# Performance work log

Measured on AMD Instinct MI355X. Metric: run time of the kernel, lower is better.

The kernel has to match this reference:

```python
import jax, jax.numpy as jnp
import numpy as np

N = 20000   # total nodes (all graphs flattened)
E = 640000  # total edges
D = 512     # num_node_features
H = 512     # hidden_channels
G = 64      # number of graphs in the batch


def setup_inputs() -> dict:
    key = jax.random.key(0)
    ks = jax.random.split(key, 12)
    s = 0.05
    return {
        "x_a": jax.random.normal(ks[0], (N, D), dtype=jnp.float32),
        "edge_index_a": jax.random.randint(ks[1], (2, E), 0, N),
        "batch_a": jnp.sort(jax.random.randint(ks[2], (N,), 0, G)),
        "x_b": jax.random.normal(ks[3], (N, D), dtype=jnp.float32),
        "edge_index_b": jax.random.randint(ks[4], (2, E), 0, N),
        "batch_b": jnp.sort(jax.random.randint(ks[5], (N,), 0, G)),
        "W1": jax.random.normal(ks[6], (D, H), dtype=jnp.float32) * s,
        "b1": jnp.zeros((H,), dtype=jnp.float32),
        "W2": jax.random.normal(ks[7], (H, H), dtype=jnp.float32) * s,
        "b2": jnp.zeros((H,), dtype=jnp.float32),
        "W3": jax.random.normal(ks[8], (H, H), dtype=jnp.float32) * s,
        "b3": jnp.zeros((H,), dtype=jnp.float32),
    }


def _gcn_conv(x, src, dst, W, b, n):
    # GCNConv with self-loops and symmetric normalization:
    # out = D^{-1/2} (A + I) D^{-1/2} X W + b,  deg_i = 1 + in_degree(i)
    h = x @ W                                                  # [n, H]
    deg = jax.ops.segment_sum(jnp.ones((src.shape[0],), h.dtype), dst,
                              num_segments=n) + 1.0            # self-loop
    dinv = jax.lax.rsqrt(deg)                                  # deg^{-1/2}
    norm = dinv[src] * dinv[dst]                               # [E]
    agg = jax.ops.segment_sum(h[src] * norm[:, None], dst, num_segments=n)
    agg = agg + h * (dinv * dinv)[:, None]                     # self-loop term
    return agg + b


def _encode(x, edge_index, batch, W1, b1, W2, b2, W3, b3):
    src, dst = edge_index[0], edge_index[1]
    n = x.shape[0]
    h = jax.nn.relu(_gcn_conv(x, src, dst, W1, b1, n))
    h = jax.nn.relu(_gcn_conv(h, src, dst, W2, b2, n))
    h = _gcn_conv(h, src, dst, W3, b3, n)
    # global mean pool over graphs
    sums = jax.ops.segment_sum(h, batch, num_segments=G)       # [G, H]
    cnts = jax.ops.segment_sum(jnp.ones((n,), h.dtype), batch, num_segments=G)
    return sums / jnp.maximum(cnts, 1.0)[:, None]


def reference(x_a, edge_index_a, batch_a, x_b, edge_index_b, batch_b,
              W1, b1, W2, b2, W3, b3):
    out_a = _encode(x_a, edge_index_a, batch_a, W1, b1, W2, b2, W3, b3)
    out_b = _encode(x_b, edge_index_b, batch_b, W1, b1, W2, b2, W3, b3)
    # torch F.pairwise_distance: ||a - b + eps||_2 with eps=1e-6
    return jnp.linalg.norm(out_a - out_b + 1e-6, axis=-1)      # [G]
```

## Files before the change

kernel.cpp:

```cpp
#include <hip/hip_runtime.h>
#include <hip/hip_fp16.h>


typedef short bf16x8 __attribute__((ext_vector_type(8)));
typedef float f32x4 __attribute__((ext_vector_type(4)));

__device__ __forceinline__ unsigned short f2bf(float f) {
    union { float f; unsigned u; } v; v.f = f;
    unsigned r = (v.u + 0x7fffu + ((v.u >> 16) & 1u)) >> 16;
    return (unsigned short)r;
}
__device__ __forceinline__ float bf2f(unsigned short h) {
    union { unsigned u; float f; } v; v.u = ((unsigned)h) << 16;
    return v.f;
}

__device__ __forceinline__ void gload16(const unsigned short* g, unsigned short* lds) {
    __builtin_amdgcn_global_load_lds(
        (const __attribute__((address_space(1))) unsigned int*)g,
        (__attribute__((address_space(3))) unsigned int*)lds, 16, 0, 0);
}


__global__ __launch_bounds__(256) void deg2_kernel(const int* __restrict__ ei_a,
                                                   const int* __restrict__ ei_b,
                                                   int* __restrict__ deg,
                                                   int n, int e) {
    int i = blockIdx.x * 256 + threadIdx.x;
    if (i >= 2 * e) return;
    if (i < e) {
        atomicAdd(&deg[ei_a[e + i]], 1);
    } else {
        atomicAdd(&deg[n + ei_b[e + (i - e)]], 1);
    }
}

__global__ __launch_bounds__(1024) void scan2_kernel(const int* __restrict__ deg_all,
                                                     int* __restrict__ rp_all,
                                                     int* __restrict__ cur_all,
                                                     float* __restrict__ dinv_all, int n) {
    int enc = blockIdx.x;
    const int* deg = deg_all + (size_t)enc * n;
    int* row_ptr = rp_all + (size_t)enc * (n + 1);
    int* cursor = cur_all + (size_t)enc * n;
    float* dinv = dinv_all + (size_t)enc * n;

    __shared__ int sums[1024];
    int t = threadIdx.x;
    int chunk = (n + 1023) >> 10;
    int beg = t * chunk;
    int end = beg + chunk;
    if (beg > n) beg = n;
    if (end > n) end = n;
    int s = 0;
    for (int i = beg; i < end; ++i) s += deg[i];
    sums[t] = s;
    __syncthreads();
    for (int off = 1; off < 1024; off <<= 1) {
        int v = (t >= off) ? sums[t - off] : 0;
        __syncthreads();
        sums[t] += v;
        __syncthreads();
    }
    int run = sums[t] - s;
    for (int i = beg; i < end; ++i) {
        row_ptr[i] = run;
        cursor[i] = run;
        dinv[i] = rsqrtf((float)deg[i] + 1.0f);
        run += deg[i];
    }
    if (t == 1023) row_ptr[n] = sums[1023];
}

__global__ __launch_bounds__(256) void fill2_kernel(const int* __restrict__ ei_a,
                                                    const int* __restrict__ ei_b,
                                                    const float* __restrict__ dinv_all,
                                                    int* __restrict__ cur_all,
                                                    int2* __restrict__ ed_all,
                                                    int n, int e) {
    int i = blockIdx.x * 256 + threadIdx.x;
    if (i >= 2 * e) return;
    int enc = (i >= e) ? 1 : 0;
    int j = i - enc * e;
    const int* ei = enc ? ei_b : ei_a;
    const float* dinv = dinv_all + (size_t)enc * n;
    int* cursor = cur_all + (size_t)enc * n;
    int2* edges = ed_all + (size_t)enc * e;
    int s = ei[j], d = ei[e + j];
    int p = atomicAdd(&cursor[d], 1);
    int2 pr;
    pr.x = s;
    pr.y = __float_as_int(dinv[s] * dinv[d]);
    edges[p] = pr;
}


__global__ __launch_bounds__(256) void ranges2_kernel(const int* __restrict__ batch_a,
                                                      const int* __restrict__ batch_b,
                                                      int* __restrict__ startA,
                                                      int* __restrict__ startB,
                                                      int n, int g) {
    int i = blockIdx.x * 256 + threadIdx.x;
    if (i >= 2 * n) return;
    int enc = (i >= n) ? 1 : 0;
    int j = i - enc * n;
    const int* batch = enc ? batch_b : batch_a;
    int* start = enc ? startB : startA;
    int b = batch[j];
    if (j == 0) {
        for (int k = 0; k <= b; ++k) start[k] = 0;
    } else {
        int pb = batch[j - 1];
        for (int k = pb + 1; k <= b; ++k) start[k] = j;
    }
    if (j == n - 1) {
        for (int k = b + 1; k <= g; ++k) start[k] = n;
    }
}


__global__ __launch_bounds__(256) void wsplit3_kernel(const float* __restrict__ W1,
                                                      const float* __restrict__ W2,
                                                      const float* __restrict__ W3,
                                                      unsigned short* __restrict__ hi_all,
                                                      unsigned short* __restrict__ lo_all) {
    __shared__ float tile[32][33];
    int layer = blockIdx.x >> 8;
    int b = blockIdx.x & 255;
    const float* W = (layer == 0) ? W1 : (layer == 1) ? W2 : W3;
    unsigned short* Wt_hi = hi_all + (size_t)layer * 512 * 512;
    unsigned short* Wt_lo = lo_all + (size_t)layer * 512 * 512;
    int k0 = (b & 15) * 32, n0 = (b >> 4) * 32;
    int t = threadIdx.x;
    int tc = t & 31, tr = t >> 5;
#pragma unroll
    for (int it = 0; it < 4; ++it)
        tile[tr + it * 8][tc] = W[(size_t)(k0 + tr + it * 8) * 512 + n0 + tc];
    __syncthreads();
#pragma unroll
    for (int it = 0; it < 4; ++it) {
        int n = tr + it * 8;
        float v = tile[tc][n];
        unsigned short hi = f2bf(v);
        unsigned short lo = f2bf(v - bf2f(hi));
        Wt_hi[(size_t)(n0 + n) * 512 + k0 + tc] = hi;
        Wt_lo[(size_t)(n0 + n) * 512 + k0 + tc] = lo;
    }
}


__global__ __launch_bounds__(256) void asplit2_kernel(const float* __restrict__ x_a,
                                                      const float* __restrict__ x_b,
                                                      unsigned short* __restrict__ A_hi,
                                                      unsigned short* __restrict__ A_lo,
                                                      int n4) {
    int i = blockIdx.x * 256 + threadIdx.x;
    if (i >= 2 * n4) return;
    float4 v = (i < n4) ? ((const float4*)x_a)[i] : ((const float4*)x_b)[i - n4];
    ushort4 h, l;
    h.x = f2bf(v.x); l.x = f2bf(v.x - bf2f(h.x));
    h.y = f2bf(v.y); l.y = f2bf(v.y - bf2f(h.y));
    h.z = f2bf(v.z); l.z = f2bf(v.z - bf2f(h.z));
    h.w = f2bf(v.w); l.w = f2bf(v.w - bf2f(h.w));
    ((ushort4*)A_hi)[i] = h;
    ((ushort4*)A_lo)[i] = l;
}


__global__ __launch_bounds__(256, 2) void gemm_mfma_kernel(const unsigned short* __restrict__ A_hi,
                                                           const unsigned short* __restrict__ A_lo,
                                                           const unsigned short* __restrict__ Bt_hi,
                                                           const unsigned short* __restrict__ Bt_lo,
                                                           __half* __restrict__ C, int M) {
    __shared__ unsigned short As_hi[2][128][32], As_lo[2][128][32];
    __shared__ unsigned short Bs_hi[2][128][32], Bs_lo[2][128][32];
    int nb = blockIdx.x & 3;
    int mb = blockIdx.x >> 2;
    int row0 = mb * 128, col0 = nb * 128;
    int t = threadIdx.x;
    int lane = t & 63, w = t >> 6;
    int wm = w >> 1, wn = w & 1;
    int r = lane & 15, g = lane >> 4;

    f32x4 acc[4][4] = {};

    int r4 = t >> 2;
    int kq = (t & 3) * 8;

    auto STAGE = [&](int buf, int k0) {
#pragma unroll
        for (int i = 0; i < 2; ++i) {
            int ldsrow = i * 64 + w * 16;
            gload16(A_hi + (size_t)(row0 + i * 64 + r4) * 512 + k0 + kq, &As_hi[buf][ldsrow][0]);
            gload16(A_lo + (size_t)(row0 + i * 64 + r4) * 512 + k0 + kq, &As_lo[buf][ldsrow][0]);
            gload16(Bt_hi + (size_t)(col0 + i * 64 + r4) * 512 + k0 + kq, &Bs_hi[buf][ldsrow][0]);
            gload16(Bt_lo + (size_t)(col0 + i * 64 + r4) * 512 + k0 + kq, &Bs_lo[buf][ldsrow][0]);
        }
    };

    STAGE(0, 0);
    __syncthreads();

    int cur = 0;
    for (int ks = 0; ks < 16; ++ks) {
        if (ks < 15) STAGE(cur ^ 1, (ks + 1) * 32);

        bf16x8 ah[4], al[4], bh[4], bl[4];
#pragma unroll
        for (int m = 0; m < 4; ++m) {
            int rr = wm * 64 + m * 16 + r;
            ah[m] = *(const bf16x8*)&As_hi[cur][rr][g * 8];
            al[m] = *(const bf16x8*)&As_lo[cur][rr][g * 8];
        }
#pragma unroll
        for (int n = 0; n < 4; ++n) {
            int cc = wn * 64 + n * 16 + r;
            bh[n] = *(const bf16x8*)&Bs_hi[cur][cc][g * 8];
            bl[n] = *(const bf16x8*)&Bs_lo[cur][cc][g * 8];
        }
#pragma unroll
        for (int m = 0; m < 4; ++m)
#pragma unroll
            for (int n = 0; n < 4; ++n) {
                acc[m][n] = __builtin_amdgcn_mfma_f32_16x16x32_bf16(al[m], bh[n], acc[m][n], 0, 0, 0);
                acc[m][n] = __builtin_amdgcn_mfma_f32_16x16x32_bf16(ah[m], bl[n], acc[m][n], 0, 0, 0);
                acc[m][n] = __builtin_amdgcn_mfma_f32_16x16x32_bf16(ah[m], bh[n], acc[m][n], 0, 0, 0);
            }
        __syncthreads();
        cur ^= 1;
    }

#pragma unroll
    for (int m = 0; m < 4; ++m)
#pragma unroll
        for (int j = 0; j < 4; ++j) {
            int rr = row0 + wm * 64 + m * 16 + g * 4 + j;
            if (rr < M) {
#pragma unroll
                for (int n = 0; n < 4; ++n)
                    C[(size_t)rr * 512 + col0 + wn * 64 + n * 16 + r] =
                        __float2half(acc[m][n][j]);
            }
        }
}


template <bool RELU, bool SPLIT>
__global__ __launch_bounds__(256) void aggregate_kernel(const __half* __restrict__ H,
                                                        const int* __restrict__ rp_all,
                                                        const int2* __restrict__ ed_all,
                                                        const float* __restrict__ dinv_all,
                                                        const float* __restrict__ bias,
                                                        float* __restrict__ X,
                                                        unsigned short* __restrict__ Xhi,
                                                        unsigned short* __restrict__ Xlo,
                                                        int n, int e) {
    int dg = blockIdx.x;
    bool isB = dg >= n;
    int d = isB ? dg - n : dg;
    const int* rp = rp_all + (isB ? (size_t)(n + 1) : 0);
    const int2* ed = ed_all + (isB ? (size_t)e : 0);
    const float* dv = dinv_all + (isB ? (size_t)n : 0);
    const __half* Hb = H + (isB ? (size_t)n * 512 : 0);

    int t = threadIdx.x;
    int beg = rp[d], end = rp[d + 1];
    float ax = 0.f, ay = 0.f;
    int j = beg;
    for (; j + 4 <= end; j += 4) {
        int2 e0 = ed[j], e1 = ed[j + 1], e2 = ed[j + 2], e3 = ed[j + 3];
        __half2 h0 = *(const __half2*)(Hb + (size_t)e0.x * 512 + t * 2);
        __half2 h1 = *(const __half2*)(Hb + (size_t)e1.x * 512 + t * 2);
        __half2 h2 = *(const __half2*)(Hb + (size_t)e2.x * 512 + t * 2);
        __half2 h3 = *(const __half2*)(Hb + (size_t)e3.x * 512 + t * 2);
        float2 f0 = __half22float2(h0), f1 = __half22float2(h1);
        float2 f2 = __half22float2(h2), f3 = __half22float2(h3);
        float w0 = __int_as_float(e0.y), w1 = __int_as_float(e1.y);
        float w2 = __int_as_float(e2.y), w3 = __int_as_float(e3.y);
        ax += w0 * f0.x + w1 * f1.x + w2 * f2.x + w3 * f3.x;
        ay += w0 * f0.y + w1 * f1.y + w2 * f2.y + w3 * f3.y;
    }
    for (; j < end; ++j) {
        int2 ej = ed[j];
        float w = __int_as_float(ej.y);
        float2 f = __half22float2(*(const __half2*)(Hb + (size_t)ej.x * 512 + t * 2));
        ax += w * f.x;
        ay += w * f.y;
    }
    float di = dv[d];
    float self = di * di;
    float2 hd = __half22float2(*(const __half2*)(Hb + (size_t)d * 512 + t * 2));
    float2 bb = *(const float2*)(bias + t * 2);
    float ox = ax + self * hd.x + bb.x;
    float oy = ay + self * hd.y + bb.y;
    if (RELU) {
        ox = fmaxf(ox, 0.f);
        oy = fmaxf(oy, 0.f);
    }
    if (SPLIT) {
        unsigned short hx = f2bf(ox), hy = f2bf(oy);
        unsigned short lx = f2bf(ox - bf2f(hx)), ly = f2bf(oy - bf2f(hy));
        *(ushort2*)(Xhi + (size_t)dg * 512 + t * 2) = make_ushort2(hx, hy);
        *(ushort2*)(Xlo + (size_t)dg * 512 + t * 2) = make_ushort2(lx, ly);
    } else {
        *(float2*)(X + (size_t)dg * 512 + t * 2) = make_float2(ox, oy);
    }
}


__global__ __launch_bounds__(256) void pool_kernel(const float* __restrict__ X,
                                                   const int* __restrict__ startA,
                                                   const int* __restrict__ startB,
                                                   float* __restrict__ pool,
                                                   int n, int gcount) {
    int g = blockIdx.x;
    bool isB = g >= gcount;
    const int* st = isB ? startB : startA;
    int gl = isB ? g - gcount : g;
    const float* Xb = X + (isB ? (size_t)n * 512 : 0);
    int t = threadIdx.x;
    int s = st[gl], e = st[gl + 1];
    float ax = 0.f, ay = 0.f;
    int i = s;
    for (; i + 2 <= e; i += 2) {
        float2 v0 = *(const float2*)(Xb + (size_t)i * 512 + t * 2);
        float2 v1 = *(const float2*)(Xb + (size_t)(i + 1) * 512 + t * 2);
        ax += v0.x + v1.x;
        ay += v0.y + v1.y;
    }
    for (; i < e; ++i) {
        float2 v = *(const float2*)(Xb + (size_t)i * 512 + t * 2);
        ax += v.x;
        ay += v.y;
    }
    float cnt = fmaxf((float)(e - s), 1.0f);
    *(float2*)(pool + (size_t)g * 512 + t * 2) = make_float2(ax / cnt, ay / cnt);
}


__global__ __launch_bounds__(64) void pdist_kernel(const float* __restrict__ pool,
                                                   float* __restrict__ out, int gcount) {
    int g = blockIdx.x;
    int t = threadIdx.x;
    const float* pa = pool + (size_t)g * 512;
    const float* pb = pool + (size_t)(gcount + g) * 512;
    float s = 0.f;
    for (int i = t; i < 512; i += 64) {
        float d = pa[i] - pb[i] + 1e-6f;
        s += d * d;
    }
#pragma unroll
    for (int off = 32; off; off >>= 1) s += __shfl_down(s, off);
    if (t == 0) out[g] = sqrtf(s);
}


extern "C" void kernel_launch(void* const* d_in, const int* in_sizes, int n_in,
                              void* d_out, int out_size, void* d_ws, size_t ws_size,
                              hipStream_t stream) {
    const float* x_a = (const float*)d_in[0];
    const int* ei_a = (const int*)d_in[1];
    const int* batch_a = (const int*)d_in[2];
    const float* x_b = (const float*)d_in[3];
    const int* ei_b = (const int*)d_in[4];
    const int* batch_b = (const int*)d_in[5];
    const float* W1 = (const float*)d_in[6];
    const float* b1 = (const float*)d_in[7];
    const float* W2 = (const float*)d_in[8];
    const float* b2 = (const float*)d_in[9];
    const float* W3 = (const float*)d_in[10];
    const float* b3 = (const float*)d_in[11];
    float* out = (float*)d_out;

    const int N = in_sizes[0] / 512;
    const int E = in_sizes[1] / 2;
    const int G = out_size;
    const int M = 2 * N;
    const int Mpad = ((M + 127) / 128) * 128;

    char* ws = (char*)d_ws;
    size_t off = 0;
    auto alloc = [&](size_t bytes) -> void* {
        void* p = ws + off;
        off = (off + bytes + 255) & ~(size_t)255;
        return p;
    };
    __half* bufH16 = (__half*)alloc((size_t)Mpad * 512 * 2);
    char* abblock = (char*)alloc((size_t)Mpad * 512 * 4);
    unsigned short* a_hi = (unsigned short*)abblock;
    unsigned short* a_lo = a_hi + (size_t)Mpad * 512;
    float* bufX = (float*)abblock;
    int* deg = (int*)alloc((size_t)2 * N * 4);
    float* dinv = (float*)alloc((size_t)2 * N * 4);
    int* rp = (int*)alloc((size_t)2 * (N + 1) * 4);
    int* cur = (int*)alloc((size_t)2 * N * 4);
    int2* ed = (int2*)alloc((size_t)2 * E * 8);
    int* startA = (int*)alloc((size_t)(G + 1) * 4);
    int* startB = (int*)alloc((size_t)(G + 1) * 4);
    float* pool = (float*)alloc((size_t)2 * G * 512 * 4);
    unsigned short* wt_hi = (unsigned short*)alloc((size_t)3 * 512 * 512 * 2);
    unsigned short* wt_lo = (unsigned short*)alloc((size_t)3 * 512 * 512 * 2);

    const int gemm_grid = 4 * (Mpad / 128);
    const int n4 = N * 512 / 4;

    wsplit3_kernel<<<768, 256, 0, stream>>>(W1, W2, W3, wt_hi, wt_lo);

    hipMemsetAsync(deg, 0, (size_t)2 * N * 4, stream);
    deg2_kernel<<<(2 * E + 255) / 256, 256, 0, stream>>>(ei_a, ei_b, deg, N, E);
    scan2_kernel<<<2, 1024, 0, stream>>>(deg, rp, cur, dinv, N);
    fill2_kernel<<<(2 * E + 255) / 256, 256, 0, stream>>>(ei_a, ei_b, dinv, cur, ed, N, E);
    ranges2_kernel<<<(2 * N + 255) / 256, 256, 0, stream>>>(batch_a, batch_b, startA, startB, N, G);

    asplit2_kernel<<<(2 * n4 + 255) / 256, 256, 0, stream>>>(x_a, x_b, a_hi, a_lo, n4);

    gemm_mfma_kernel<<<gemm_grid, 256, 0, stream>>>(a_hi, a_lo, wt_hi, wt_lo, bufH16, M);
    aggregate_kernel<true, true><<<M, 256, 0, stream>>>(bufH16, rp, ed, dinv, b1,
                                                        bufX, a_hi, a_lo, N, E);
    gemm_mfma_kernel<<<gemm_grid, 256, 0, stream>>>(a_hi, a_lo, wt_hi + (size_t)512 * 512,
                                                    wt_lo + (size_t)512 * 512, bufH16, M);
    aggregate_kernel<true, true><<<M, 256, 0, stream>>>(bufH16, rp, ed, dinv, b2,
                                                        bufX, a_hi, a_lo, N, E);
    gemm_mfma_kernel<<<gemm_grid, 256, 0, stream>>>(a_hi, a_lo, wt_hi + (size_t)2 * 512 * 512,
                                                    wt_lo + (size_t)2 * 512 * 512, bufH16, M);
    aggregate_kernel<false, false><<<M, 256, 0, stream>>>(bufH16, rp, ed, dinv, b3,
                                                          bufX, a_hi, a_lo, N, E);

    pool_kernel<<<2 * G, 256, 0, stream>>>(bufX, startA, startB, pool, N, G);
    pdist_kernel<<<G, 64, 0, stream>>>(pool, out, G);
}
```

Before: 1.116 ms.

## Retile GEMM to 64-row blocks spanning all 512 columns, drop double buffering

The split-bf16 MFMA GEMM now gives each block 64 rows and the full 512 output columns, with each wave owning 128 columns. A is loaded once per row block instead of once per column block, and the grid shrinks to about M/64 blocks. The LDS double buffering is removed, so loads are no longer overlapped with MFMA work and there is a sync before compute. The B tile grows to 64 KB of LDS per k-step, which lowers occupancy, and a 128-element accumulator per thread raises register pressure.

```diff
diff --git a/kernel.cpp b/kernel.cpp
--- a/kernel.cpp
+++ b/kernel.cpp
@@ -172,74 +172,59 @@
                                                            const unsigned short* __restrict__ Bt_hi,
                                                            const unsigned short* __restrict__ Bt_lo,
                                                            __half* __restrict__ C, int M) {
-    __shared__ unsigned short As_hi[2][128][32], As_lo[2][128][32];
-    __shared__ unsigned short Bs_hi[2][128][32], Bs_lo[2][128][32];
-    int nb = blockIdx.x & 3;
-    int mb = blockIdx.x >> 2;
-    int row0 = mb * 128, col0 = nb * 128;
+    __shared__ unsigned short As_hi[64][32], As_lo[64][32];
+    __shared__ unsigned short Bs_hi[512][32], Bs_lo[512][32];
+    int row0 = blockIdx.x * 64;
     int t = threadIdx.x;
     int lane = t & 63, w = t >> 6;
-    int wm = w >> 1, wn = w & 1;
     int r = lane & 15, g = lane >> 4;
 
-    f32x4 acc[4][4] = {};
-
-    int r4 = t >> 2;
+    f32x4 acc[4][8] = {};
+
+    int ar = t >> 2;
     int kq = (t & 3) * 8;
 
-    auto STAGE = [&](int buf, int k0) {
-#pragma unroll
-        for (int i = 0; i < 2; ++i) {
+    for (int k0 = 0; k0 < 512; k0 += 32) {
+        gload16(A_hi + (size_t)(row0 + ar) * 512 + k0 + kq, &As_hi[w * 16][0]);
+        gload16(A_lo + (size_t)(row0 + ar) * 512 + k0 + kq, &As_lo[w * 16][0]);
+#pragma unroll
+        for (int i = 0; i < 8; ++i) {
             int ldsrow = i * 64 + w * 16;
-            gload16(A_hi + (size_t)(row0 + i * 64 + r4) * 512 + k0 + kq, &As_hi[buf][ldsrow][0]);
-            gload16(A_lo + (size_t)(row0 + i * 64 + r4) * 512 + k0 + kq, &As_lo[buf][ldsrow][0]);
-            gload16(Bt_hi + (size_t)(col0 + i * 64 + r4) * 512 + k0 + kq, &Bs_hi[buf][ldsrow][0]);
-            gload16(Bt_lo + (size_t)(col0 + i * 64 + r4) * 512 + k0 + kq, &Bs_lo[buf][ldsrow][0]);
+            gload16(Bt_hi + (size_t)(i * 64 + ar) * 512 + k0 + kq, &Bs_hi[ldsrow][0]);
+            gload16(Bt_lo + (size_t)(i * 64 + ar) * 512 + k0 + kq, &Bs_lo[ldsrow][0]);
         }
-    };
-
-    STAGE(0, 0);
-    __syncthreads();
-
-    int cur = 0;
-    for (int ks = 0; ks < 16; ++ks) {
-        if (ks < 15) STAGE(cur ^ 1, (ks + 1) * 32);
-
-        bf16x8 ah[4], al[4], bh[4], bl[4];
+        __syncthreads();
+
+        bf16x8 ah[4], al[4];
 #pragma unroll
         for (int m = 0; m < 4; ++m) {
-            int rr = wm * 64 + m * 16 + r;
-            ah[m] = *(const bf16x8*)&As_hi[cur][rr][g * 8];
-            al[m] = *(const bf16x8*)&As_lo[cur][rr][g * 8];
+            ah[m] = *(const bf16x8*)&As_hi[m * 16 + r][g * 8];
+            al[m] = *(const bf16x8*)&As_lo[m * 16 + r][g * 8];
         }
 #pragma unroll
-        for (int n = 0; n < 4; ++n) {
-            int cc = wn * 64 + n * 16 + r;
-            bh[n] = *(const bf16x8*)&Bs_hi[cur][cc][g * 8];
-            bl[n] = *(const bf16x8*)&Bs_lo[cur][cc][g * 8];
+        for (int n = 0; n < 8; ++n) {
+            int cc = w * 128 + n * 16 + r;
+            bf16x8 bh = *(const bf16x8*)&Bs_hi[cc][g * 8];
+            bf16x8 bl = *(const bf16x8*)&Bs_lo[cc][g * 8];
+#pragma unroll
+            for (int m = 0; m < 4; ++m) {
+                acc[m][n] = __builtin_amdgcn_mfma_f32_16x16x32_bf16(al[m], bh, acc[m][n], 0, 0, 0);
+                acc[m][n] = __builtin_amdgcn_mfma_f32_16x16x32_bf16(ah[m], bl, acc[m][n], 0, 0, 0);
+                acc[m][n] = __builtin_amdgcn_mfma_f32_16x16x32_bf16(ah[m], bh, acc[m][n], 0, 0, 0);
+            }
         }
-#pragma unroll
-        for (int m = 0; m < 4; ++m)
-#pragma unroll
-            for (int n = 0; n < 4; ++n) {
-                acc[m][n] = __builtin_amdgcn_mfma_f32_16x16x32_bf16(al[m], bh[n], acc[m][n], 0, 0, 0);
-                acc[m][n] = __builtin_amdgcn_mfma_f32_16x16x32_bf16(ah[m], bl[n], acc[m][n], 0, 0, 0);
-                acc[m][n] = __builtin_amdgcn_mfma_f32_16x16x32_bf16(ah[m], bh[n], acc[m][n], 0, 0, 0);
-            }
         __syncthreads();
-        cur ^= 1;
     }
 
 #pragma unroll
     for (int m = 0; m < 4; ++m)
 #pragma unroll
         for (int j = 0; j < 4; ++j) {
-            int rr = row0 + wm * 64 + m * 16 + g * 4 + j;
+            int rr = row0 + m * 16 + g * 4 + j;
             if (rr < M) {
 #pragma unroll
-                for (int n = 0; n < 4; ++n)
-                    C[(size_t)rr * 512 + col0 + wn * 64 + n * 16 + r] =
-                        __float2half(acc[m][n][j]);
+                for (int n = 0; n < 8; ++n)
+                    C[(size_t)rr * 512 + w * 128 + n * 16 + r] = __float2half(acc[m][n][j]);
             }
         }
 }
@@ -401,7 +386,7 @@
     unsigned short* wt_hi = (unsigned short*)alloc((size_t)3 * 512 * 512 * 2);
     unsigned short* wt_lo = (unsigned short*)alloc((size_t)3 * 512 * 512 * 2);
 
-    const int gemm_grid = 4 * (Mpad / 128);
+    const int gemm_grid = (M + 63) / 64;
     const int n4 = N * 512 / 4;
 
     wsplit3_kernel<<<768, 256, 0, stream>>>(W1, W2, W3, wt_hi, wt_lo);
```

Result: no change. 1.099 ms (-1.5%).
